# Kernel optimization log

Hardware: AMD Instinct MI355X
Metric: run time of the kernel (lower is better)

Reference implementation:

```python
import jax, jax.numpy as jnp
import numpy as np

B, N, T, C, D, K, DEG = 4, 2000, 12, 64, 64, 3, 8
E = N * DEG  # 16000 edges per dilation graph


def setup_inputs() -> dict:
    key = jax.random.key(0)
    ks = jax.random.split(key, 6)
    input_feature = jax.random.normal(ks[0], (B, N, T, C), jnp.float32)
    src = jax.random.randint(ks[1], (K, E), 0, N, jnp.int32)
    # every node receives exactly DEG in-edges -> softmax segments never empty
    dst = jnp.broadcast_to(jnp.repeat(jnp.arange(N, dtype=jnp.int32), DEG), (K, E))
    edges = jnp.stack([src, dst], axis=1)  # [K, 2, E]
    W_mlp = jax.random.normal(ks[2], (C, D), jnp.float32) / np.sqrt(C).astype(np.float32)
    b_mlp = jnp.zeros((D,), jnp.float32)
    W_attn = jax.random.normal(ks[3], (2 * D, D), jnp.float32) / np.sqrt(2 * D).astype(np.float32)
    b_attn = jnp.zeros((D,), jnp.float32)
    weight = jax.random.normal(ks[4], (K, 1), jnp.float32) * 0.05  # init_weight()
    return {"input_feature": input_feature, "W_mlp": W_mlp, "b_mlp": b_mlp,
            "W_attn": W_attn, "b_attn": b_attn, "weight": weight, "edges": edges}


def _gcn(feats, src, dst, W_attn, b_attn, n_nodes):
    # feats: [N, B, T, D] (node-major, as after transpose(0,1) in torch)
    h_src = feats[src]  # [E, B, T, D] gather
    h_dst = feats[dst]  # [E, B, T, D]
    # per-edge channel-wise attention logits: [E, B, T, D]
    scores = jnp.concatenate([h_src, h_dst], axis=-1) @ W_attn + b_attn
    # segment (per-dst-node) softmax over incoming edges, numerically stable
    m = jax.ops.segment_max(scores, dst, num_segments=n_nodes)  # [N, B, T, D]
    ex = jnp.exp(scores - m[dst])
    denom = jax.ops.segment_sum(ex, dst, num_segments=n_nodes)
    num = jax.ops.segment_sum(ex * h_src, dst, num_segments=n_nodes)
    return num / denom  # [N, B, T, D]


def reference(input_feature, W_mlp, b_mlp, W_attn, b_attn, weight, edges):
    n_nodes = input_feature.shape[1]
    feats = jnp.einsum('bntc,cd->bntd', input_feature, W_mlp) + b_mlp
    feats = jnp.swapaxes(feats, 0, 1)  # [N, B, T, D]
    result = jnp.zeros_like(feats)
    for i in range(edges.shape[0]):  # small fixed num_kernel loop
        src, dst = edges[i, 0], edges[i, 1]
        result = result + weight[i] * _gcn(feats, src, dst, W_attn, b_attn, n_nodes)
    out = jax.nn.leaky_relu(jnp.swapaxes(result, 0, 1), 0.01)
    return out + input_feature  # residual is Identity since in_dim == out_dim
```

## Files before the change

kernel.cpp:

```cpp
#include <hip/hip_runtime.h>
#include <hip/hip_bf16.h>
#include <stdint.h>

#define B_ 4
#define N_ 2000
#define T_ 12
#define D_ 64
#define K_ 3
#define DEG_ 8
#define E_ (N_*DEG_)
#define ROWS_ (B_*N_*T_)
#define NT_ (N_*T_)
#define EPN_ (B_*T_*D_)
#define V4PB_ (T_*D_/4)
#define ROWBYTES_ (EPN_*4)
#define LOG2E_ 1.4426950408889634f

typedef __attribute__((ext_vector_type(8))) short short8v;
typedef __attribute__((ext_vector_type(4))) float f32x4;

__device__ __forceinline__ uint32_t f32_to_bf16_bits(float x) {
    uint32_t u = __float_as_uint(x);
    return (u + 0x7FFFu + ((u >> 16) & 1u)) >> 16;
}
__device__ __forceinline__ uint32_t pack2(float p, float f) {
    return (f32_to_bf16_bits(p) << 16) | f32_to_bf16_bits(f);
}
__device__ __forceinline__ short8v cvt8(float4 lo, float4 hi) {
    short8v af;
    af[0] = (short)f32_to_bf16_bits(lo.x);
    af[1] = (short)f32_to_bf16_bits(lo.y);
    af[2] = (short)f32_to_bf16_bits(lo.z);
    af[3] = (short)f32_to_bf16_bits(lo.w);
    af[4] = (short)f32_to_bf16_bits(hi.x);
    af[5] = (short)f32_to_bf16_bits(hi.y);
    af[6] = (short)f32_to_bf16_bits(hi.z);
    af[7] = (short)f32_to_bf16_bits(hi.w);
    return af;
}

__global__ void prep_kernel(const float* __restrict__ Wm,
                            const float* __restrict__ Wa,
                            const float* __restrict__ bm,
                            uint16_t* __restrict__ WBf,
                            float* __restrict__ bpp) {
    const int blk  = blockIdx.x;
    const int lane = threadIdx.x;
    if (blk < 16) {
        const int tile = blk >> 1, s = blk & 1;
        const int r = lane & 15, q = lane >> 4;
        const int c = tile*16 + r;
        uint16_t o[8];
        #pragma unroll
        for (int e = 0; e < 8; ++e) {
            const int k = s*32 + q*8 + e;
            float v;
            if (c < 64) {
                v = Wm[k*64 + c];
            } else {
                v = 0.f;
                #pragma unroll
                for (int j = 0; j < 64; ++j) v += Wm[k*64 + j] * Wa[j*64 + (c - 64)];
                v *= LOG2E_;
            }
            o[e] = (uint16_t)f32_to_bf16_bits(v);
        }
        *(uint4*)(WBf + (size_t)(blk*64 + lane)*8) = *(const uint4*)o;
    } else {
        float s = 0.f;
        #pragma unroll
        for (int e = 0; e < 64; ++e) s += bm[e] * Wa[e*64 + lane];
        bpp[lane] = s * LOG2E_;
    }
}

__launch_bounds__(256)
__global__ void mlp_mfma(const float* __restrict__ X,
                         const uint16_t* __restrict__ WBf,
                         const float* __restrict__ bm,
                         const float* __restrict__ bpp,
                         uint32_t* __restrict__ packed) {
    const int t    = threadIdx.x;
    const int wave = t >> 6, lane = t & 63;
    const int r    = lane & 15, q = lane >> 4;

    const int row0 = blockIdx.x*128 + wave*32;
    const int gR0  = row0 + r;
    const int gR1  = row0 + 16 + r;

    const float* xp0 = X + (size_t)gR0*64 + q*8;
    const float* xp1 = X + (size_t)gR1*64 + q*8;
    const float4 a00 = *(const float4*)(xp0);
    const float4 a01 = *(const float4*)(xp0 + 4);
    const float4 a02 = *(const float4*)(xp0 + 32);
    const float4 a03 = *(const float4*)(xp0 + 36);
    const float4 a10 = *(const float4*)(xp1);
    const float4 a11 = *(const float4*)(xp1 + 4);
    const float4 a12 = *(const float4*)(xp1 + 32);
    const float4 a13 = *(const float4*)(xp1 + 36);

    short8v wfrag[8][2];
    #pragma unroll
    for (int tile = 0; tile < 8; ++tile)
        #pragma unroll
        for (int s = 0; s < 2; ++s)
            wfrag[tile][s] = *(const short8v*)(WBf + (size_t)((tile*2+s)*64 + lane)*8);

    f32x4 acc0[8], acc1[8];
    #pragma unroll
    for (int tile = 0; tile < 8; ++tile) {
        acc0[tile] = (f32x4){0.f,0.f,0.f,0.f};
        acc1[tile] = (f32x4){0.f,0.f,0.f,0.f};
    }

    {
        const short8v af = cvt8(a00, a01);
        #pragma unroll
        for (int tile = 0; tile < 8; ++tile)
            acc0[tile] = __builtin_amdgcn_mfma_f32_16x16x32_bf16(wfrag[tile][0], af, acc0[tile], 0, 0, 0);
    }
    {
        const short8v af = cvt8(a02, a03);
        #pragma unroll
        for (int tile = 0; tile < 8; ++tile)
            acc0[tile] = __builtin_amdgcn_mfma_f32_16x16x32_bf16(wfrag[tile][1], af, acc0[tile], 0, 0, 0);
    }
    {
        const short8v af = cvt8(a10, a11);
        #pragma unroll
        for (int tile = 0; tile < 8; ++tile)
            acc1[tile] = __builtin_amdgcn_mfma_f32_16x16x32_bf16(wfrag[tile][0], af, acc1[tile], 0, 0, 0);
    }
    {
        const short8v af = cvt8(a12, a13);
        #pragma unroll
        for (int tile = 0; tile < 8; ++tile)
            acc1[tile] = __builtin_amdgcn_mfma_f32_16x16x32_bf16(wfrag[tile][1], af, acc1[tile], 0, 0, 0);
    }

    #pragma unroll
    for (int rt = 0; rt < 2; ++rt) {
        const int gR = rt ? gR1 : gR0;
        const f32x4* acc = rt ? acc1 : acc0;
        const int b  = gR / NT_;
        const int rm = gR - b*NT_;
        const int n  = rm / T_;
        const int tt = rm - n*T_;
        uint32_t* dstrow = packed + (size_t)n*EPN_ + b*(T_*D_) + tt*D_;
        #pragma unroll
        for (int tf = 0; tf < 4; ++tf) {
            const int d0 = tf*16 + q*4;
            const float4 bm4 = *(const float4*)&bm[d0];
            const float4 bp4 = *(const float4*)&bpp[d0];
            uint4 u;
            u.x = pack2(__builtin_amdgcn_exp2f(acc[tf+4][0] + bp4.x), acc[tf][0] + bm4.x);
            u.y = pack2(__builtin_amdgcn_exp2f(acc[tf+4][1] + bp4.y), acc[tf][1] + bm4.y);
            u.z = pack2(__builtin_amdgcn_exp2f(acc[tf+4][2] + bp4.z), acc[tf][2] + bm4.z);
            u.w = pack2(__builtin_amdgcn_exp2f(acc[tf+4][3] + bp4.w), acc[tf][3] + bm4.w);
            *(uint4*)(dstrow + d0) = u;
        }
    }
}

__launch_bounds__(128, 3)
__global__ void gcn_kernel(const uint32_t* __restrict__ packed,
                           const float* __restrict__ input,
                           const int* __restrict__ edges,
                           const float* __restrict__ weight,
                           float* __restrict__ out) {
    const uint32_t wgid = blockIdx.x;
    const uint32_t xcd  = wgid & 7;
    const uint32_t slot = wgid >> 3;
    const uint32_t vw   = xcd * 1500u + slot;
    const int ss   = (int)(vw / 1000u);
    const int pair = (int)(vw - (uint32_t)ss * 1000u);

    const int wv = __builtin_amdgcn_readfirstlane(threadIdx.x >> 6);
    const int n  = pair*2 + wv;
    const int t  = threadIdx.x & 63;

    const int vv = ss*64 + t;
    const int b  = vv / V4PB_;
    const int r4 = vv - b*V4PB_;
    const size_t off4 = (size_t)b*(NT_*D_/4) + (size_t)n*V4PB_ + r4;

    int srcs[24];
    #pragma unroll
    for (int k = 0; k < K_; ++k) {
        const int4 e0 = *(const int4*)(edges + (size_t)k*(2*E_) + n*DEG_);
        const int4 e1 = *(const int4*)(edges + (size_t)k*(2*E_) + n*DEG_ + 4);
        srcs[k*8+0]=e0.x; srcs[k*8+1]=e0.y; srcs[k*8+2]=e0.z; srcs[k*8+3]=e0.w;
        srcs[k*8+4]=e1.x; srcs[k*8+5]=e1.y; srcs[k*8+6]=e1.z; srcs[k*8+7]=e1.w;
    }

    const float4 inv = ((const float4*)input)[off4];
#define GLOAD(i) const uint4 pu##i = *(const uint4*)((const char*)packed \
        + (size_t)((uint32_t)srcs[i] * (uint32_t)ROWBYTES_) + (size_t)vv * 16)
    GLOAD(0);  GLOAD(1);  GLOAD(2);  GLOAD(3);  GLOAD(4);  GLOAD(5);
    GLOAD(6);  GLOAD(7);  GLOAD(8);  GLOAD(9);  GLOAD(10); GLOAD(11);
    GLOAD(12); GLOAD(13); GLOAD(14); GLOAD(15); GLOAD(16); GLOAD(17);
    GLOAD(18); GLOAD(19); GLOAD(20); GLOAD(21); GLOAD(22); GLOAD(23);
#undef GLOAD
    __builtin_amdgcn_sched_barrier(0);

    const uint4 pu[24] = {pu0,pu1,pu2,pu3,pu4,pu5,pu6,pu7,pu8,pu9,pu10,pu11,
                          pu12,pu13,pu14,pu15,pu16,pu17,pu18,pu19,pu20,pu21,pu22,pu23};

    float acc[4] = {0.f, 0.f, 0.f, 0.f};
    #pragma unroll
    for (int k = 0; k < K_; ++k) {
        const float wk = weight[k];
        #pragma unroll
        for (int qq = 0; qq < 4; ++qq) {
            float s = 0.f, num = 0.f;
            #pragma unroll
            for (int j = 0; j < 8; ++j) {
                const uint4 pv = pu[k*8 + j];
                const uint32_t u = (qq == 0) ? pv.x : (qq == 1) ? pv.y
                                 : (qq == 2) ? pv.z : pv.w;
                const float p = __uint_as_float(u & 0xFFFF0000u);
                const float f = __uint_as_float(u << 16);
                s += p;
                num = fmaf(p, f, num);
            }
            acc[qq] += wk * num * __builtin_amdgcn_rcpf(s);
        }
    }

    float4 o;
    o.x = (acc[0] > 0.f ? acc[0] : 0.01f*acc[0]) + inv.x;
    o.y = (acc[1] > 0.f ? acc[1] : 0.01f*acc[1]) + inv.y;
    o.z = (acc[2] > 0.f ? acc[2] : 0.01f*acc[2]) + inv.z;
    o.w = (acc[3] > 0.f ? acc[3] : 0.01f*acc[3]) + inv.w;
    ((float4*)out)[off4] = o;
}

extern "C" void kernel_launch(void* const* d_in, const int* in_sizes, int n_in,
                              void* d_out, int out_size, void* d_ws, size_t ws_size,
                              hipStream_t stream) {
    const float* input  = (const float*)d_in[0];
    const float* Wm     = (const float*)d_in[1];
    const float* bm     = (const float*)d_in[2];
    const float* Wa     = (const float*)d_in[3];
    const float* weight = (const float*)d_in[5];
    const int*   edges  = (const int*)d_in[6];
    float* out = (float*)d_out;
    uint32_t* packed = (uint32_t*)d_ws;

    uint16_t* WBf = (uint16_t*)d_out;
    float*    bpp = (float*)d_out + 4096;

    hipLaunchKernelGGL(prep_kernel, dim3(17), dim3(64), 0, stream, Wm, Wa, bm, WBf, bpp);
    hipLaunchKernelGGL(mlp_mfma, dim3(ROWS_/128), dim3(256), 0, stream,
                       input, WBf, bm, bpp, packed);
    hipLaunchKernelGGL(gcn_kernel, dim3(12000), dim3(128), 0, stream,
                       packed, input, edges, weight, out);
}
```

Before: 50.36 us.

## Store attention exp weights as FP8 in chunked 12-byte slots to cut gather bytes

The packed per-node intermediate now stores the exponentiated attention weight as FP8 (via cvt_pk_fp8) next to BF16 features. Each 4-channel slot shrinks from 16 to 12 bytes, and the layout changes to chunks of 64 slots per node so each gcn thread gathers a 12-byte vector. This cuts the bytes moved by the gather-heavy gcn kernel. The occupancy hint is raised to 4 waves per SIMD. FP8 softmax weights lower accuracy and may push errors close to the tolerance.

```diff
diff --git a/kernel.cpp b/kernel.cpp
--- a/kernel.cpp
+++ b/kernel.cpp
@@ -11,20 +11,19 @@
 #define E_ (N_*DEG_)
 #define ROWS_ (B_*N_*T_)
 #define NT_ (N_*T_)
-#define EPN_ (B_*T_*D_)
 #define V4PB_ (T_*D_/4)
-#define ROWBYTES_ (EPN_*4)
+#define SLOTB_ 12
+#define CHUNKB_ (64*SLOTB_)
 #define LOG2E_ 1.4426950408889634f
 
 typedef __attribute__((ext_vector_type(8))) short short8v;
 typedef __attribute__((ext_vector_type(4))) float f32x4;
+typedef __attribute__((ext_vector_type(2))) float f32x2;
+typedef __attribute__((ext_vector_type(3))) unsigned int u32x3;
 
 __device__ __forceinline__ uint32_t f32_to_bf16_bits(float x) {
     uint32_t u = __float_as_uint(x);
     return (u + 0x7FFFu + ((u >> 16) & 1u)) >> 16;
-}
-__device__ __forceinline__ uint32_t pack2(float p, float f) {
-    return (f32_to_bf16_bits(p) << 16) | f32_to_bf16_bits(f);
 }
 __device__ __forceinline__ short8v cvt8(float4 lo, float4 hi) {
     short8v af;
@@ -79,7 +78,7 @@
                          const uint16_t* __restrict__ WBf,
                          const float* __restrict__ bm,
                          const float* __restrict__ bpp,
-                         uint32_t* __restrict__ packed) {
+                         char* __restrict__ packed) {
     const int t    = threadIdx.x;
     const int wave = t >> 6, lane = t & 63;
     const int r    = lane & 15, q = lane >> 4;
@@ -146,24 +145,35 @@
         const int rm = gR - b*NT_;
         const int n  = rm / T_;
         const int tt = rm - n*T_;
-        uint32_t* dstrow = packed + (size_t)n*EPN_ + b*(T_*D_) + tt*D_;
+        const int vbase = b*192 + tt*16;
         #pragma unroll
         for (int tf = 0; tf < 4; ++tf) {
             const int d0 = tf*16 + q*4;
             const float4 bm4 = *(const float4*)&bm[d0];
             const float4 bp4 = *(const float4*)&bpp[d0];
-            uint4 u;
-            u.x = pack2(__builtin_amdgcn_exp2f(acc[tf+4][0] + bp4.x), acc[tf][0] + bm4.x);
-            u.y = pack2(__builtin_amdgcn_exp2f(acc[tf+4][1] + bp4.y), acc[tf][1] + bm4.y);
-            u.z = pack2(__builtin_amdgcn_exp2f(acc[tf+4][2] + bp4.z), acc[tf][2] + bm4.z);
-            u.w = pack2(__builtin_amdgcn_exp2f(acc[tf+4][3] + bp4.w), acc[tf][3] + bm4.w);
-            *(uint4*)(dstrow + d0) = u;
+            const float f0 = acc[tf][0] + bm4.x;
+            const float f1 = acc[tf][1] + bm4.y;
+            const float f2 = acc[tf][2] + bm4.z;
+            const float f3 = acc[tf][3] + bm4.w;
+            const float p0 = __builtin_amdgcn_exp2f(acc[tf+4][0] + bp4.x);
+            const float p1 = __builtin_amdgcn_exp2f(acc[tf+4][1] + bp4.y);
+            const float p2 = __builtin_amdgcn_exp2f(acc[tf+4][2] + bp4.z);
+            const float p3 = __builtin_amdgcn_exp2f(acc[tf+4][3] + bp4.w);
+            int pw = __builtin_amdgcn_cvt_pk_fp8_f32(p0, p1, 0, false);
+            pw     = __builtin_amdgcn_cvt_pk_fp8_f32(p2, p3, pw, true);
+            const uint32_t f01 = (f32_to_bf16_bits(f1) << 16) | f32_to_bf16_bits(f0);
+            const uint32_t f23 = (f32_to_bf16_bits(f3) << 16) | f32_to_bf16_bits(f2);
+            const int vv = vbase + tf*4 + q;
+            char* slot = packed + ((size_t)(vv >> 6)*2000 + n)*CHUNKB_ + (size_t)(vv & 63)*SLOTB_;
+            uint2 fw; fw.x = f01; fw.y = f23;
+            *(uint2*)slot = fw;
+            *(uint32_t*)(slot + 8) = (uint32_t)pw;
         }
     }
 }
 
-__launch_bounds__(128, 3)
-__global__ void gcn_kernel(const uint32_t* __restrict__ packed,
+__launch_bounds__(128, 4)
+__global__ void gcn_kernel(const char* __restrict__ packed,
                            const float* __restrict__ input,
                            const int* __restrict__ edges,
                            const float* __restrict__ weight,
@@ -194,8 +204,8 @@
     }
 
     const float4 inv = ((const float4*)input)[off4];
-#define GLOAD(i) const uint4 pu##i = *(const uint4*)((const char*)packed \
-        + (size_t)((uint32_t)srcs[i] * (uint32_t)ROWBYTES_) + (size_t)vv * 16)
+    const char* pbase = packed + (size_t)((uint32_t)(ss*2000))*CHUNKB_ + (size_t)t*SLOTB_;
+#define GLOAD(i) const u32x3 g##i = *(const u32x3*)(pbase + (size_t)(uint32_t)srcs[i]*CHUNKB_)
     GLOAD(0);  GLOAD(1);  GLOAD(2);  GLOAD(3);  GLOAD(4);  GLOAD(5);
     GLOAD(6);  GLOAD(7);  GLOAD(8);  GLOAD(9);  GLOAD(10); GLOAD(11);
     GLOAD(12); GLOAD(13); GLOAD(14); GLOAD(15); GLOAD(16); GLOAD(17);
@@ -203,28 +213,33 @@
 #undef GLOAD
     __builtin_amdgcn_sched_barrier(0);
 
-    const uint4 pu[24] = {pu0,pu1,pu2,pu3,pu4,pu5,pu6,pu7,pu8,pu9,pu10,pu11,
-                          pu12,pu13,pu14,pu15,pu16,pu17,pu18,pu19,pu20,pu21,pu22,pu23};
+    const u32x3 g[24] = {g0,g1,g2,g3,g4,g5,g6,g7,g8,g9,g10,g11,
+                         g12,g13,g14,g15,g16,g17,g18,g19,g20,g21,g22,g23};
 
     float acc[4] = {0.f, 0.f, 0.f, 0.f};
     #pragma unroll
     for (int k = 0; k < K_; ++k) {
         const float wk = weight[k];
-        #pragma unroll
-        for (int qq = 0; qq < 4; ++qq) {
-            float s = 0.f, num = 0.f;
-            #pragma unroll
-            for (int j = 0; j < 8; ++j) {
-                const uint4 pv = pu[k*8 + j];
-                const uint32_t u = (qq == 0) ? pv.x : (qq == 1) ? pv.y
-                                 : (qq == 2) ? pv.z : pv.w;
-                const float p = __uint_as_float(u & 0xFFFF0000u);
-                const float f = __uint_as_float(u << 16);
-                s += p;
-                num = fmaf(p, f, num);
-            }
-            acc[qq] += wk * num * __builtin_amdgcn_rcpf(s);
+        float s0=0.f,s1=0.f,s2=0.f,s3=0.f;
+        float n0=0.f,n1=0.f,n2=0.f,n3=0.f;
+        #pragma unroll
+        for (int j = 0; j < 8; ++j) {
+            const u32x3 gv = g[k*8 + j];
+            const f32x2 pA = __builtin_amdgcn_cvt_pk_f32_fp8((int)gv[2], false);
+            const f32x2 pB = __builtin_amdgcn_cvt_pk_f32_fp8((int)gv[2], true);
+            const float f0 = __uint_as_float(gv[0] << 16);
+            const float f1 = __uint_as_float(gv[0] & 0xFFFF0000u);
+            const float f2 = __uint_as_float(gv[1] << 16);
+            const float f3 = __uint_as_float(gv[1] & 0xFFFF0000u);
+            s0 += pA[0]; n0 = fmaf(pA[0], f0, n0);
+            s1 += pA[1]; n1 = fmaf(pA[1], f1, n1);
+            s2 += pB[0]; n2 = fmaf(pB[0], f2, n2);
+            s3 += pB[1]; n3 = fmaf(pB[1], f3, n3);
         }
+        acc[0] += wk * n0 * __builtin_amdgcn_rcpf(s0);
+        acc[1] += wk * n1 * __builtin_amdgcn_rcpf(s1);
+        acc[2] += wk * n2 * __builtin_amdgcn_rcpf(s2);
+        acc[3] += wk * n3 * __builtin_amdgcn_rcpf(s3);
     }
 
     float4 o;
@@ -245,7 +260,7 @@
     const float* weight = (const float*)d_in[5];
     const int*   edges  = (const int*)d_in[6];
     float* out = (float*)d_out;
-    uint32_t* packed = (uint32_t*)d_ws;
+    char* packed = (char*)d_ws;
 
     uint16_t* WBf = (uint16_t*)d_out;
     float*    bpp = (float*)d_out + 4096;
```

Measured after the change: 47.07 us. 1.07x faster.
